# Performance work log

Measured on AMD Instinct MI355X. Metric: run time of the kernel, lower is better.

## Reference

```python
import math
import jax, jax.numpy as jnp
import numpy as np

B, D, T = 4, 512, 1024
H, DH, FF, K = 8, 64, 4, 31
NB, MD = 320, 800  # num_buckets, max_distance
ATTN_SCALE = 32.0


def setup_inputs() -> dict:
    key = jax.random.key(0)
    ks = jax.random.split(key, 16)
    n = lambda k, shape, s=0.02: jax.random.normal(k, shape, jnp.float32) * s
    return {
        "x": jax.random.normal(ks[0], (B, D, T), jnp.float32),
        "ff1_w1": n(ks[1], (D, FF * D)), "ff1_b1": jnp.zeros((FF * D,)),
        "ff1_w2": n(ks[2], (FF * D, D)), "ff1_b2": jnp.zeros((D,)),
        "qkv_w": n(ks[3], (D, 3 * D)), "qkv_b": jnp.zeros((3 * D,)),
        "out_w": n(ks[4], (D, D)), "out_b": jnp.zeros((D,)),
        "gn1_g": jnp.ones((D,)), "gn1_b": jnp.zeros((D,)),
        "pw1_w": n(ks[5], (D, 2 * D)), "pw1_b": jnp.zeros((2 * D,)),
        "dw_w": n(ks[6], (D, K)), "dw_b": jnp.zeros((D,)),
        "gn2_g": jnp.ones((D,)), "gn2_b": jnp.zeros((D,)),
        "pw2_w": n(ks[7], (D, D)), "pw2_b": jnp.zeros((D,)),
        "ff2_w1": n(ks[8], (D, FF * D)), "ff2_b1": jnp.zeros((FF * D,)),
        "ff2_w2": n(ks[9], (FF * D, D)), "ff2_b2": jnp.zeros((D,)),
        "rel_embed": n(ks[10], (NB, H), 1.0),
        "gate_u": n(ks[11], (H, DH)), "gate_w": n(ks[12], (H, DH)),
        "gate_scale": jnp.ones((H,)),
    }


def _rel_buckets(seq_len):
    # WavLM-style bucketization of relative positions (int, no grad).
    pos = jnp.arange(seq_len)
    rel = pos[None, :] - pos[:, None]                 # [T, T]
    half = NB // 2
    small = half // 2
    sign = (rel >= 0).astype(jnp.int32)
    a = jnp.abs(rel)
    is_small = a < small
    ac = jnp.maximum(a, 1)
    log_ratio = jnp.log(ac.astype(jnp.float32) / small) / math.log(MD / small)
    log_pos = small + (log_ratio * (half - small)).astype(jnp.int32)  # trunc toward 0, matches .long()
    log_pos = jnp.minimum(log_pos, half - 1)
    bucket = jnp.where(is_small, a, log_pos) + sign * half
    return jnp.clip(bucket, 0, NB - 1)


def _ffn(h, w1, b1, w2, b2):
    return jax.nn.gelu(h @ w1 + b1, approximate=False) @ w2 + b2


def _groupnorm1(h, g, b):  # GroupNorm(1, C) over [B, C, T]
    m = h.mean(axis=(1, 2), keepdims=True)
    v = h.var(axis=(1, 2), keepdims=True)
    return (h - m) / jnp.sqrt(v + 1e-5) * g[None, :, None] + b[None, :, None]


def reference(x, ff1_w1, ff1_b1, ff1_w2, ff1_b2, qkv_w, qkv_b, out_w, out_b,
              gn1_g, gn1_b, pw1_w, pw1_b, dw_w, dw_b, gn2_g, gn2_b, pw2_w, pw2_b,
              ff2_w1, ff2_b1, ff2_w2, ff2_b2, rel_embed, gate_u, gate_w, gate_scale):
    b_, d_, t_ = x.shape
    s = jnp.transpose(x, (0, 2, 1))                     # [B, T, D]
    s = s + 0.5 * _ffn(s, ff1_w1, ff1_b1, ff1_w2, ff1_b2)

    qkv = (s @ qkv_w + qkv_b).reshape(b_, t_, 3, H, DH)
    q = jnp.transpose(qkv[:, :, 0], (0, 2, 1, 3))       # [B, H, T, DH]
    k = jnp.transpose(qkv[:, :, 1], (0, 2, 1, 3))
    v = jnp.transpose(qkv[:, :, 2], (0, 2, 1, 3))

    scores = jnp.einsum('bhtd,bhsd->bhts', q / ATTN_SCALE, k)
    scores = (scores - scores.max(axis=-1, keepdims=True)) * ATTN_SCALE / math.sqrt(DH)

    # gated relative-position bias
    buckets = _rel_buckets(t_)                          # [T, T] int
    d = jnp.transpose(rel_embed[buckets], (2, 0, 1))[None]   # [1, H, T, T]
    g_upd = jax.nn.sigmoid(jnp.einsum('bhtd,hd->bht', q, gate_u))[..., None]
    g_rst = jax.nn.sigmoid(jnp.einsum('bhtd,hd->bht', q, gate_w))[..., None]
    r_tilde = gate_scale[None, :, None, None] * g_rst * d
    r = d + g_upd * d + (1 - g_upd) * r_tilde           # [B, H, T, T]

    probs = jax.nn.softmax(scores + r, axis=-1)
    attn = jnp.einsum('bhts,bhsd->bthd', probs, v).reshape(b_, t_, d_)
    s = s + attn @ out_w + out_b

    # conv module
    c = jnp.transpose(s, (0, 2, 1))                     # [B, D, T]
    h = _groupnorm1(c, gn1_g, gn1_b)
    h = jnp.einsum('bct,co->bot', h, pw1_w) + pw1_b[None, :, None]   # pointwise 1x1
    h_a, h_b = jnp.split(h, 2, axis=1)
    h = h_a * jax.nn.sigmoid(h_b)                       # GLU(dim=1)
    h = jax.lax.conv_general_dilated(
        h, dw_w[:, None, :], window_strides=(1,), padding=[(K // 2, K // 2)],
        dimension_numbers=('NCH', 'OIH', 'NCH'), feature_group_count=d_
    ) + dw_b[None, :, None]                             # depthwise conv
    h = _groupnorm1(h, gn2_g, gn2_b)
    h = jax.nn.silu(h)
    h = jnp.einsum('bct,co->bot', h, pw2_w) + pw2_b[None, :, None]
    c = c + h

    st = jnp.transpose(c, (0, 2, 1))
    st = st + 0.5 * _ffn(st, ff2_w1, ff2_b1, ff2_w2, ff2_b2)
    return jnp.transpose(st, (0, 2, 1))                 # [B, D, T]
```

## Files before the change

kernel.cpp:

```cpp
#include <hip/hip_runtime.h>
#include <hip/hip_bf16.h>
#include <math.h>

#define B_ 4
#define D_ 512
#define T_ 1024
#define H_ 8
#define FFD 2048

typedef unsigned short u16;
typedef short s16x8 __attribute__((ext_vector_type(8)));
typedef float f32x4 __attribute__((ext_vector_type(4)));

__device__ inline float sigm(float x){ return 1.f/(1.f+expf(-x)); }
__device__ inline float gelu_exact(float x){ return 0.5f*x*(1.f+erff(x*0.70710678118654752440f)); }
__device__ inline u16 f2b(float f){
  __hip_bfloat16 h = __float2bfloat16(f);
  return *reinterpret_cast<u16*>(&h);
}
__device__ inline float b2f(u16 u){ return __uint_as_float(((unsigned)u)<<16); }

__device__ inline void gl_lds16(const void* g, void* l) {
  __builtin_amdgcn_global_load_lds(
      (const __attribute__((address_space(1))) void*)g,
      (__attribute__((address_space(3))) void*)l, 16, 0, 0);
}

__global__ __launch_bounds__(256) void k_wt(const float* __restrict__ w, u16* __restrict__ wt, int K, int N) {
  __shared__ float tile[32][33];
  int n0 = blockIdx.x*32, k0 = blockIdx.y*32;
  int c = threadIdx.x & 31, r = threadIdx.x >> 5;
  for (int rr = r; rr < 32; rr += 8)
    tile[rr][c] = w[(size_t)(k0+rr)*N + n0 + c];
  __syncthreads();
  for (int rr = r; rr < 32; rr += 8)
    wt[(size_t)(n0+rr)*K + k0 + c] = f2b(tile[c][rr]);
}

__global__ __launch_bounds__(256) void k_wt_glu(const float* __restrict__ w, u16* __restrict__ wt, int K, int N) {
  __shared__ float tile[32][33];
  int n0 = blockIdx.x*32, k0 = blockIdx.y*32;
  int c = threadIdx.x & 31, r = threadIdx.x >> 5;
  for (int rr = r; rr < 32; rr += 8)
    tile[rr][c] = w[(size_t)(k0+rr)*N + n0 + c];
  __syncthreads();
  for (int rr = r; rr < 32; rr += 8) {
    int nr = n0 + rr;
    int np = (nr < 512) ? (nr*2) : ((nr-512)*2 + 1);
    wt[(size_t)np*K + k0 + c] = f2b(tile[c][rr]);
  }
}

__global__ void k_dwt(const float* __restrict__ w, float* __restrict__ wdt) {
  int idx = blockIdx.x*256 + threadIdx.x;
  if (idx < 31*512) {
    int k = idx >> 9, d = idx & 511;
    wdt[idx] = w[d*31 + k];
  }
}

__global__ __launch_bounds__(256) void k_xin(const float* __restrict__ x, float* __restrict__ sf, u16* __restrict__ sb) {
  __shared__ float tile[32][33];
  int b = blockIdx.z;
  int d0 = blockIdx.y * 32;
  int t0 = blockIdx.x * 32;
  int c = threadIdx.x & 31, r = threadIdx.x >> 5;
  for (int rr = r; rr < 32; rr += 8)
    tile[rr][c] = x[((size_t)(b*D_ + d0 + rr))*T_ + t0 + c];
  __syncthreads();
  for (int rr = r; rr < 32; rr += 8) {
    float v = tile[c][rr];
    size_t o = ((size_t)(b*T_ + t0 + rr))*D_ + d0 + c;
    sf[o] = v; sb[o] = f2b(v);
  }
}

__global__ __launch_bounds__(256) void k_transpose_out(const float* __restrict__ s, float* __restrict__ o) {
  __shared__ float tile[32][33];
  int b = blockIdx.z;
  int t0 = blockIdx.y * 32;
  int d0 = blockIdx.x * 32;
  int c = threadIdx.x & 31, r = threadIdx.x >> 5;
  for (int rr = r; rr < 32; rr += 8)
    tile[rr][c] = s[((size_t)(b*T_ + t0 + rr))*D_ + d0 + c];
  __syncthreads();
  for (int rr = r; rr < 32; rr += 8)
    o[((size_t)(b*D_ + d0 + rr))*T_ + t0 + c] = tile[c][rr];
}

template<int BM>
__global__ __launch_bounds__(256) void k_gemm_mfma(
    const u16* __restrict__ A, const u16* __restrict__ Wt,
    const float* __restrict__ bias, const float* __restrict__ res, float rscale,
    float* __restrict__ outf, u16* __restrict__ outb,
    u16* __restrict__ qd, u16* __restrict__ kd, u16* __restrict__ vd,
    u16* __restrict__ glub, float2* __restrict__ gnp, float* __restrict__ partf,
    int M, int N, int K, int kLen, int act)
{
  constexpr int MFR = BM/32;
  __shared__ u16 Ab[BM*64];
  __shared__ u16 Bb[128*64];
  int tid = threadIdx.x;
  int w = tid >> 6, lane = tid & 63;
  int lr = lane & 15, lk = lane >> 4;
  int wm = w >> 1, wn = w & 1;
  int m0 = blockIdx.y * BM, n0 = blockIdx.x * 128;
  int kbeg = partf ? blockIdx.z * kLen : 0;
  int kend = partf ? kbeg + kLen : K;
  f32x4 acc[MFR][4] = {};

  for (int kt = kbeg; kt < kend; kt += 64) {
    #pragma unroll
    for (int i = 0; i < MFR; ++i) {
      int slot = (w*MFR + i)*64 + lane;
      int r = slot >> 3, sc = slot & 7;
      int cc = sc ^ (r & 7);
      gl_lds16(A + (size_t)(m0 + r)*K + kt + cc*8, (char*)Ab + (size_t)(w*MFR+i)*1024);
    }
    #pragma unroll
    for (int i = 0; i < 4; ++i) {
      int slot = (w*4 + i)*64 + lane;
      int r = slot >> 3, sc = slot & 7;
      int cc = sc ^ (r & 7);
      gl_lds16(Wt + (size_t)(n0 + r)*K + kt + cc*8, (char*)Bb + (size_t)(w*4+i)*1024);
    }
    __syncthreads();
    #pragma unroll
    for (int ks = 0; ks < 2; ++ks) {
      s16x8 af[MFR], bfv[4];
      #pragma unroll
      for (int m = 0; m < MFR; ++m) {
        int r = wm*(BM/2) + m*16 + lr;
        int sl = (ks*4 + lk) ^ (r & 7);
        af[m] = *(const s16x8*)(Ab + r*64 + sl*8);
      }
      #pragma unroll
      for (int n = 0; n < 4; ++n) {
        int r = wn*64 + n*16 + lr;
        int sl = (ks*4 + lk) ^ (r & 7);
        bfv[n] = *(const s16x8*)(Bb + r*64 + sl*8);
      }
      #pragma unroll
      for (int m = 0; m < MFR; ++m)
        #pragma unroll
        for (int n = 0; n < 4; ++n)
          acc[m][n] = __builtin_amdgcn_mfma_f32_16x16x32_bf16(af[m], bfv[n], acc[m][n], 0, 0, 0);
    }
    __syncthreads();
  }

  if (partf) {
    float* pp = partf + (size_t)blockIdx.z * M * N;
    #pragma unroll
    for (int m = 0; m < MFR; ++m)
      #pragma unroll
      for (int n = 0; n < 4; ++n)
        #pragma unroll
        for (int r2 = 0; r2 < 4; ++r2) {
          int row = m0 + wm*(BM/2) + m*16 + lk*4 + r2;
          int col = n0 + wn*64 + n*16 + lr;
          pp[(size_t)row*N + col] = acc[m][n][r2];
        }
    return;
  }

  float psum = 0.f, psq = 0.f;
  #pragma unroll
  for (int m = 0; m < MFR; ++m) {
    #pragma unroll
    for (int n = 0; n < 4; ++n) {
      #pragma unroll
      for (int r2 = 0; r2 < 4; ++r2) {
        int row = m0 + wm*(BM/2) + m*16 + lk*4 + r2;
        int col = n0 + wn*64 + n*16 + lr;
        if (glub) {
          float vv = acc[m][n][r2] + bias[(col&1)*512 + (col>>1)];
          float pv = __shfl_xor(vv, 1);
          if ((col & 1) == 0)
            glub[(size_t)row*512 + (col>>1)] = f2b(vv * sigm(pv));
        } else {
          float vv = acc[m][n][r2] + bias[col];
          if (act) vv = gelu_exact(vv);
          size_t off = (size_t)row * N + col;
          if (res)  vv = res[off] + rscale * vv;
          if (outf) outf[off] = vv;
          if (outb) outb[off] = f2b(vv);
          if (qd) {
            int part = col >> 9, h = (col >> 6) & 7, dh = col & 63;
            int b = row >> 10, t = row & (T_-1);
            u16* dst = part == 0 ? qd : (part == 1 ? kd : vd);
            dst[(((size_t)(b*H_ + h))*T_ + t)*64 + dh] = f2b(vv);
          }
          psum += vv; psq += vv*vv;
        }
      }
    }
  }
  if (gnp) {
    float* r1 = (float*)Ab;
    float* r2s = (float*)Bb;
    __syncthreads();
    r1[tid] = psum; r2s[tid] = psq;
    __syncthreads();
    for (int off = 128; off; off >>= 1) {
      if (tid < off) { r1[tid] += r1[tid+off]; r2s[tid] += r2s[tid+off]; }
      __syncthreads();
    }
    if (tid == 0) {
      int bb = m0 >> 10;
      int mloc = (m0 >> (BM==64 ? 6 : 7)) & ((1024/BM) - 1);
      int idx = bb*(1024/BM)*4 + mloc*4 + (n0 >> 7);
      gnp[idx] = make_float2(r1[0], r2s[0]);
    }
  }
}

__global__ __launch_bounds__(256) void k_combine(
    const float4* __restrict__ p, const float* __restrict__ bias,
    const float4* __restrict__ res, float rscale,
    float4* __restrict__ outf, u16* __restrict__ outb)
{
  size_t i = (size_t)blockIdx.x*256 + threadIdx.x;
  int c4 = (i & 127) << 2;
  float4 a = p[i];
  float4 b = p[i + (size_t)(B_*T_)*128];
  float4 bs = *(const float4*)(bias + c4);
  float4 r = res[i];
  float4 v;
  v.x = r.x + rscale*(a.x + b.x + bs.x);
  v.y = r.y + rscale*(a.y + b.y + bs.y);
  v.z = r.z + rscale*(a.z + b.z + bs.z);
  v.w = r.w + rscale*(a.w + b.w + bs.w);
  if (outf) outf[i] = v;
  if (outb) {
    ushort4 u; u.x = f2b(v.x); u.y = f2b(v.y); u.z = f2b(v.z); u.w = f2b(v.w);
    *(ushort4*)(outb + i*4) = u;
  }
}

__global__ void k_rb(const float* __restrict__ rel_embed, float* __restrict__ rbg) {
  int idx = blockIdx.x*256 + threadIdx.x;
  int h = idx >> 11, j = idx & 2047;
  if (j >= 2047) { rbg[idx] = 0.f; return; }
  int rel = j - 1023;
  int sign = rel >= 0 ? 1 : 0;
  int a = rel >= 0 ? rel : -rel;
  int bkt;
  if (a < 80) bkt = a;
  else {
    float lr = logf((float)a / 80.f) / 2.30258509299404568402f;
    int lp = 80 + (int)(lr * 80.f);
    bkt = lp < 159 ? lp : 159;
  }
  bkt += sign*160;
  rbg[idx] = rel_embed[bkt*H_ + h];
}

__global__ __launch_bounds__(256) void k_vt(const u16* __restrict__ vb, u16* __restrict__ vtb) {
  __shared__ u16 tl[64][65];
  int blk = blockIdx.x;
  int tt0 = (blk & 15) * 64;
  size_t bh = (size_t)(blk >> 4);
  int tid = threadIdx.x;
  #pragma unroll
  for (int i = 0; i < 4; ++i) {
    int idx = i*256 + tid;
    int t = idx >> 4, d0 = (idx & 15) * 4;
    *(ushort4*)&tl[t][d0] = *(const ushort4*)(vb + (bh*T_ + tt0 + t)*64 + d0);
  }
  __syncthreads();
  #pragma unroll
  for (int i = 0; i < 4; ++i) {
    int idx = i*256 + tid;
    int dh = idx >> 4, t4 = (idx & 15) * 4;
    ushort4 o;
    o.x = tl[t4+0][dh]; o.y = tl[t4+1][dh]; o.z = tl[t4+2][dh]; o.w = tl[t4+3][dh];
    *(ushort4*)(vtb + (bh*64 + dh)*T_ + tt0 + t4) = o;
  }
}

__global__ __launch_bounds__(256) void k_attn3(
    const u16* __restrict__ qb, const u16* __restrict__ kb, const u16* __restrict__ vtb,
    const float* __restrict__ rbg,
    const float* __restrict__ gu, const float* __restrict__ gw, const float* __restrict__ gs,
    u16* __restrict__ outb)
{
  __shared__ u16 Kl[64*64];
  __shared__ u16 Vtl[64*64];
  __shared__ u16 Pl[64*64];
  __shared__ float rb[2048];
  __shared__ float cf[64];
  int blk = blockIdx.x;
  int qt = blk & 15;
  int h  = (blk >> 4) & 7;
  int b  = blk >> 7;
  int tid = threadIdx.x;
  int w = tid >> 6, lane = tid & 63;
  int lr = lane & 15, lk = lane >> 4;
  int g = lane >> 4;
  int t0 = qt * 64;
  size_t bh = (size_t)(b*H_ + h);

  for (int j = tid; j < 2048; j += 256) rb[j] = rbg[h*2048 + j];
  if (tid < 64) {
    const u16* qrow = qb + (bh*T_ + t0 + tid)*64;
    float vu = 0.f, vw = 0.f;
    for (int kk2 = 0; kk2 < 64; ++kk2) {
      float qv = b2f(qrow[kk2]);
      vu += qv * gu[h*64+kk2];
      vw += qv * gw[h*64+kk2];
    }
    float g1 = sigm(vu), g2 = sigm(vw);
    cf[tid] = 1.f + g1 + (1.f-g1)*gs[h]*g2;
  }
  const u16* qbase = qb + (bh*T_ + t0 + w*16 + lr)*64;
  s16x8 qa0 = *(const s16x8*)(qbase + lk*8);
  s16x8 qa1 = *(const s16x8*)(qbase + 32 + lk*8);

  f32x4 O[4] = {};
  float mcur[4] = {-1e30f,-1e30f,-1e30f,-1e30f};
  float lsum[4] = {0.f,0.f,0.f,0.f};
  const f32x4 zero = {0.f,0.f,0.f,0.f};
  __syncthreads();

  for (int kt = 0; kt < 16; ++kt) {
    #pragma unroll
    for (int i = 0; i < 2; ++i) {
      int slot = (i*4 + w)*64 + lane;
      int r = slot >> 3, scc = slot & 7;
      int cc = scc ^ (r & 7);
      gl_lds16(kb  + (bh*T_ + kt*64 + r)*64 + cc*8, (char*)Kl  + (i*4+w)*1024);
      gl_lds16(vtb + (bh*64 + r)*T_ + kt*64 + cc*8, (char*)Vtl + (i*4+w)*1024);
    }
    __syncthreads();
    f32x4 sc[4];
    #pragma unroll
    for (int n = 0; n < 4; ++n) {
      int row = n*16 + lr;
      int c0 = (0*4 + lk) ^ (row & 7);
      int c1 = (1*4 + lk) ^ (row & 7);
      s16x8 kb0 = *(const s16x8*)(Kl + row*64 + c0*8);
      s16x8 kb1 = *(const s16x8*)(Kl + row*64 + c1*8);
      f32x4 t = __builtin_amdgcn_mfma_f32_16x16x32_bf16(qa0, kb0, zero, 0, 0, 0);
      sc[n]   = __builtin_amdgcn_mfma_f32_16x16x32_bf16(qa1, kb1, t, 0, 0, 0);
    }
    float tmax[4];
    #pragma unroll
    for (int r2 = 0; r2 < 4; ++r2) {
      int q_local = w*16 + g*4 + r2;
      float cfv = cf[q_local];
      int qabs = t0 + q_local;
      float mx = -1e30f;
      #pragma unroll
      for (int n = 0; n < 4; ++n) {
        int sabs = kt*64 + n*16 + lr;
        float v = sc[n][r2]*0.125f + cfv * rb[sabs - qabs + 1023];
        sc[n][r2] = v;
        mx = fmaxf(mx, v);
      }
      tmax[r2] = mx;
    }
    #pragma unroll
    for (int mk = 1; mk < 16; mk <<= 1)
      #pragma unroll
      for (int r2 = 0; r2 < 4; ++r2)
        tmax[r2] = fmaxf(tmax[r2], __shfl_xor(tmax[r2], mk));
    float scl[4], psum[4];
    #pragma unroll
    for (int r2 = 0; r2 < 4; ++r2) {
      float mnew = fmaxf(mcur[r2], tmax[r2]);
      scl[r2] = __expf(mcur[r2] - mnew);
      mcur[r2] = mnew;
      int q_local = w*16 + g*4 + r2;
      float ps = 0.f;
      #pragma unroll
      for (int n = 0; n < 4; ++n) {
        float e = __expf(sc[n][r2] - mnew);
        ps += e;
        int s_local = n*16 + lr;
        Pl[q_local*64 + (((s_local>>3) ^ (q_local&7))<<3) + (s_local&7)] = f2b(e);
      }
      psum[r2] = ps;
    }
    #pragma unroll
    for (int mk = 1; mk < 16; mk <<= 1)
      #pragma unroll
      for (int r2 = 0; r2 < 4; ++r2)
        psum[r2] += __shfl_xor(psum[r2], mk);
    #pragma unroll
    for (int r2 = 0; r2 < 4; ++r2) lsum[r2] = lsum[r2]*scl[r2] + psum[r2];
    #pragma unroll
    for (int n = 0; n < 4; ++n)
      #pragma unroll
      for (int r2 = 0; r2 < 4; ++r2)
        O[n][r2] *= scl[r2];
    __syncthreads();
    int qrow = w*16 + lr;
    int pc0 = (0*4 + lk) ^ (qrow & 7), pc1 = (1*4 + lk) ^ (qrow & 7);
    s16x8 pa0 = *(const s16x8*)(Pl + qrow*64 + pc0*8);
    s16x8 pa1 = *(const s16x8*)(Pl + qrow*64 + pc1*8);
    #pragma unroll
    for (int n = 0; n < 4; ++n) {
      int dh = n*16 + lr;
      int c0 = (0*4 + lk) ^ (dh & 7), c1 = (1*4 + lk) ^ (dh & 7);
      s16x8 vb0 = *(const s16x8*)(Vtl + dh*64 + c0*8);
      s16x8 vb1 = *(const s16x8*)(Vtl + dh*64 + c1*8);
      O[n] = __builtin_amdgcn_mfma_f32_16x16x32_bf16(pa0, vb0, O[n], 0, 0, 0);
      O[n] = __builtin_amdgcn_mfma_f32_16x16x32_bf16(pa1, vb1, O[n], 0, 0, 0);
    }
    __syncthreads();
  }
  float inv[4];
  #pragma unroll
  for (int r2 = 0; r2 < 4; ++r2) inv[r2] = 1.f / lsum[r2];
  #pragma unroll
  for (int n = 0; n < 4; ++n)
    #pragma unroll
    for (int r2 = 0; r2 < 4; ++r2) {
      int q = t0 + w*16 + g*4 + r2;
      int dh = n*16 + lr;
      outb[((size_t)(b*T_) + q)*512 + h*64 + dh] = f2b(O[n][r2]*inv[r2]);
    }
}

__global__ __launch_bounds__(256) void k_dwconv2(
    const u16* __restrict__ g, const float* __restrict__ wdt,
    const float* __restrict__ bias, float* __restrict__ o, float2* __restrict__ part)
{
  int b = blockIdx.z, tg = blockIdx.y;
  int ch = blockIdx.x*256 + threadIdx.x;
  int t0 = tg*16;
  float wk[31];
  #pragma unroll
  for (int k = 0; k < 31; ++k) wk[k] = wdt[k*512 + ch];
  float win[46];
  const u16* gb = g + ((size_t)b*T_)*512 + ch;
  #pragma unroll
  for (int j = 0; j < 46; ++j) {
    int tt = t0 + j - 15;
    win[j] = (tt >= 0 && tt < T_) ? b2f(gb[(size_t)tt*512]) : 0.f;
  }
  float bv = bias[ch];
  float bsum = 0.f, bsq = 0.f;
  float* ob = o + ((size_t)b*T_ + t0)*512 + ch;
  #pragma unroll
  for (int j = 0; j < 16; ++j) {
    float acc = bv;
    #pragma unroll
    for (int k = 0; k < 31; ++k) acc += win[j+k]*wk[k];
    ob[(size_t)j*512] = acc;
    bsum += acc; bsq += acc*acc;
  }
  __shared__ float rs[256], rq[256];
  rs[threadIdx.x] = bsum; rq[threadIdx.x] = bsq; __syncthreads();
  for (int off = 128; off; off >>= 1) {
    if (threadIdx.x < off) { rs[threadIdx.x] += rs[threadIdx.x+off]; rq[threadIdx.x] += rq[threadIdx.x+off]; }
    __syncthreads();
  }
  if (threadIdx.x == 0) part[b*128 + tg*2 + blockIdx.x] = make_float2(rs[0], rq[0]);
}

__global__ void k_gn_final(const float2* __restrict__ part, float2* __restrict__ stats, int n) {
  int b = blockIdx.x;
  float s = 0.f, s2 = 0.f;
  for (int i = threadIdx.x; i < n; i += 64) {
    float2 p = part[b*n + i];
    s += p.x; s2 += p.y;
  }
  for (int off = 32; off; off >>= 1) { s += __shfl_down(s, off); s2 += __shfl_down(s2, off); }
  if (threadIdx.x == 0) {
    float cnt = (float)(D_*T_);
    float mean = s/cnt;
    float var = s2/cnt - mean*mean;
    stats[b] = make_float2(mean, rsqrtf(var + 1e-5f));
  }
}

__global__ void k_gn_apply(const float* __restrict__ x, const float2* __restrict__ stats,
                           const float* __restrict__ g, const float* __restrict__ bta,
                           u16* __restrict__ o, int silu_flag)
{
  size_t idx = (size_t)blockIdx.x*256 + threadIdx.x;
  int dd = idx & (D_-1);
  int b = (int)(idx >> 19);
  float2 st = stats[b];
  float v = (x[idx]-st.x)*st.y*g[dd] + bta[dd];
  if (silu_flag) v = v*sigm(v);
  o[idx] = f2b(v);
}

extern "C" void kernel_launch(void* const* d_in, const int* in_sizes, int n_in,
                              void* d_out, int out_size, void* d_ws, size_t ws_size,
                              hipStream_t stream)
{
  const float* x      = (const float*)d_in[0];
  const float* ff1_w1 = (const float*)d_in[1];
  const float* ff1_b1 = (const float*)d_in[2];
  const float* ff1_w2 = (const float*)d_in[3];
  const float* ff1_b2 = (const float*)d_in[4];
  const float* qkv_w  = (const float*)d_in[5];
  const float* qkv_b  = (const float*)d_in[6];
  const float* out_w  = (const float*)d_in[7];
  const float* out_b  = (const float*)d_in[8];
  const float* gn1_g  = (const float*)d_in[9];
  const float* gn1_b  = (const float*)d_in[10];
  const float* pw1_w  = (const float*)d_in[11];
  const float* pw1_b  = (const float*)d_in[12];
  const float* dw_w   = (const float*)d_in[13];
  const float* dw_b   = (const float*)d_in[14];
  const float* gn2_g  = (const float*)d_in[15];
  const float* gn2_b  = (const float*)d_in[16];
  const float* pw2_w  = (const float*)d_in[17];
  const float* pw2_b  = (const float*)d_in[18];
  const float* ff2_w1 = (const float*)d_in[19];
  const float* ff2_b1 = (const float*)d_in[20];
  const float* ff2_w2 = (const float*)d_in[21];
  const float* ff2_b2 = (const float*)d_in[22];
  const float* rel_embed = (const float*)d_in[23];
  const float* gate_u = (const float*)d_in[24];
  const float* gate_w = (const float*)d_in[25];
  const float* gate_scale = (const float*)d_in[26];

  char* ws = (char*)d_ws;
  const size_t MB = (size_t)1 << 20;
  float* s0f  = (float*)(ws + 0*MB);
  u16*   s0b  = (u16*)  (ws + 8*MB);
  u16*   h1b  = (u16*)  (ws + 12*MB);
  float* Sf   = (float*)(ws + 28*MB);
  u16*   Sb   = (u16*)  (ws + 36*MB);
  u16*   qbb  = (u16*)  (ws + 40*MB);
  u16*   kbb  = (u16*)  (ws + 44*MB);
  u16*   vbb  = (u16*)  (ws + 48*MB);
  u16*   vtb  = (u16*)  (ws + 52*MB);
  float* S2f  = (float*)(ws + 0*MB);
  u16*   attb = (u16*)  (ws + 8*MB);
  u16*   gn1b = (u16*)  (ws + 36*MB);
  u16*   glub = (u16*)  (ws + 56*MB);
  float* dcf  = (float*)(ws + 28*MB);
  u16*   gn2b = (u16*)  (ws + 36*MB);
  float* S3f  = (float*)(ws + 40*MB);
  u16*   S3b  = (u16*)  (ws + 48*MB);
  u16*   h3b  = (u16*)  (ws + 12*MB);
  float* Sout = (float*)(ws + 28*MB);
  float* PK1  = (float*)(ws + 40*MB);
  float* PK2  = (float*)(ws + 48*MB);
  u16* ff1w1t = (u16*)(ws + 64*MB);
  u16* ff1w2t = (u16*)(ws + 66*MB);
  u16* qkvt   = (u16*)(ws + 68*MB);
  u16* outt   = (u16*)(ws + 70*MB);
  u16* pw1t   = (u16*)(ws + 72*MB);
  u16* pw2t   = (u16*)(ws + 74*MB);
  u16* ff2w1t = (u16*)(ws + 76*MB);
  u16* ff2w2t = (u16*)(ws + 78*MB);
  float* rbg  = (float*)(ws + 80*MB);
  float* wdt  = (float*)(ws + 81*MB);
  float2* part1 = (float2*)(ws + 84*MB);
  float2* part2 = (float2*)(ws + 84*MB + 8192);
  float2* st1   = (float2*)(ws + 84*MB + 16384);
  float2* st2   = (float2*)(ws + 84*MB + 16384 + 64);

  const int M = B_*T_;
  dim3 blk(256);

  k_wt<<<dim3(FFD/32, D_/32), blk, 0, stream>>>(ff1_w1, ff1w1t, D_, FFD);
  k_wt<<<dim3(D_/32, FFD/32), blk, 0, stream>>>(ff1_w2, ff1w2t, FFD, D_);
  k_wt<<<dim3(1536/32, D_/32), blk, 0, stream>>>(qkv_w, qkvt, D_, 1536);
  k_wt<<<dim3(D_/32, D_/32), blk, 0, stream>>>(out_w, outt, D_, D_);
  k_wt_glu<<<dim3(1024/32, D_/32), blk, 0, stream>>>(pw1_w, pw1t, D_, 1024);
  k_wt<<<dim3(D_/32, D_/32), blk, 0, stream>>>(pw2_w, pw2t, D_, D_);
  k_wt<<<dim3(FFD/32, D_/32), blk, 0, stream>>>(ff2_w1, ff2w1t, D_, FFD);
  k_wt<<<dim3(D_/32, FFD/32), blk, 0, stream>>>(ff2_w2, ff2w2t, FFD, D_);
  k_rb<<<dim3(64), blk, 0, stream>>>(rel_embed, rbg);
  k_dwt<<<dim3(62), blk, 0, stream>>>(dw_w, wdt);

  k_xin<<<dim3(T_/32, D_/32, B_), blk, 0, stream>>>(x, s0f, s0b);

  k_gemm_mfma<128><<<dim3(FFD/128, M/128), blk, 0, stream>>>(s0b, ff1w1t, ff1_b1, nullptr, 0.f,
      nullptr, h1b, nullptr, nullptr, nullptr, nullptr, nullptr, nullptr, M, FFD, D_, 0, 1);
  k_gemm_mfma<64><<<dim3(D_/128, M/64, 2), blk, 0, stream>>>(h1b, ff1w2t, nullptr, nullptr, 0.f,
      nullptr, nullptr, nullptr, nullptr, nullptr, nullptr, nullptr, PK1, M, D_, FFD, 1024, 0);
  k_combine<<<dim3((M*128)/256), blk, 0, stream>>>((const float4*)PK1, ff1_b2, (const float4*)s0f, 0.5f,
      (float4*)Sf, Sb);
  k_gemm_mfma<64><<<dim3(1536/128, M/64), blk, 0, stream>>>(Sb, qkvt, qkv_b, nullptr, 0.f,
      nullptr, nullptr, qbb, kbb, vbb, nullptr, nullptr, nullptr, M, 1536, D_, 0, 0);
  k_vt<<<dim3(B_*H_*16), blk, 0, stream>>>(vbb, vtb);
  k_attn3<<<dim3(B_*H_*16), blk, 0, stream>>>(qbb, kbb, vtb, rbg, gate_u, gate_w, gate_scale, attb);
  k_gemm_mfma<64><<<dim3(D_/128, M/64), blk, 0, stream>>>(attb, outt, out_b, Sf, 1.f,
      S2f, nullptr, nullptr, nullptr, nullptr, nullptr, part1, nullptr, M, D_, D_, 0, 0);
  k_gn_final<<<dim3(B_), dim3(64), 0, stream>>>(part1, st1, 64);
  k_gn_apply<<<dim3((M*D_)/256), blk, 0, stream>>>(S2f, st1, gn1_g, gn1_b, gn1b, 0);
  k_gemm_mfma<64><<<dim3(1024/128, M/64), blk, 0, stream>>>(gn1b, pw1t, pw1_b, nullptr, 0.f,
      nullptr, nullptr, nullptr, nullptr, nullptr, glub, nullptr, nullptr, M, 1024, D_, 0, 0);
  k_dwconv2<<<dim3(2, T_/16, B_), blk, 0, stream>>>(glub, wdt, dw_b, dcf, part2);
  k_gn_final<<<dim3(B_), dim3(64), 0, stream>>>(part2, st2, 128);
  k_gn_apply<<<dim3((M*D_)/256), blk, 0, stream>>>(dcf, st2, gn2_g, gn2_b, gn2b, 1);
  k_gemm_mfma<64><<<dim3(D_/128, M/64), blk, 0, stream>>>(gn2b, pw2t, pw2_b, S2f, 1.f,
      S3f, S3b, nullptr, nullptr, nullptr, nullptr, nullptr, nullptr, M, D_, D_, 0, 0);
  k_gemm_mfma<128><<<dim3(FFD/128, M/128), blk, 0, stream>>>(S3b, ff2w1t, ff2_b1, nullptr, 0.f,
      nullptr, h3b, nullptr, nullptr, nullptr, nullptr, nullptr, nullptr, M, FFD, D_, 0, 1);
  k_gemm_mfma<64><<<dim3(D_/128, M/64, 2), blk, 0, stream>>>(h3b, ff2w2t, nullptr, nullptr, 0.f,
      nullptr, nullptr, nullptr, nullptr, nullptr, nullptr, nullptr, PK2, M, D_, FFD, 1024, 0);
  k_combine<<<dim3((M*128)/256), blk, 0, stream>>>((const float4*)PK2, ff2_b2, (const float4*)S3f, 0.5f,
      (float4*)Sout, nullptr);
  k_transpose_out<<<dim3(D_/32, T_/32, B_), blk, 0, stream>>>(Sout, (float*)d_out);
}
```

Baseline: 439.3 us.

## Merge prep kernels, fold GN finalize into apply, use 64x64 GEMM tiles

Eleven setup launches (weight transposes, relative-bias table, depthwise weight transpose, input transpose) are merged into a single k_prep kernel that dispatches on block index. The two GroupNorm finalize kernels are removed, and every k_gn_apply block now reduces the 128 partial stats itself, which repeats that small reduction in each block. The smaller GEMMs move from 64x128 to 64x64 tiles, doubling the grid to fill more CUs at the cost of less operand reuse per block.

```diff
diff --git a/kernel.cpp b/kernel.cpp
--- a/kernel.cpp
+++ b/kernel.cpp
@@ -26,53 +26,93 @@
       (__attribute__((address_space(3))) void*)l, 16, 0, 0);
 }
 
-__global__ __launch_bounds__(256) void k_wt(const float* __restrict__ w, u16* __restrict__ wt, int K, int N) {
-  __shared__ float tile[32][33];
-  int n0 = blockIdx.x*32, k0 = blockIdx.y*32;
-  int c = threadIdx.x & 31, r = threadIdx.x >> 5;
-  for (int rr = r; rr < 32; rr += 8)
-    tile[rr][c] = w[(size_t)(k0+rr)*N + n0 + c];
-  __syncthreads();
-  for (int rr = r; rr < 32; rr += 8)
-    wt[(size_t)(n0+rr)*K + k0 + c] = f2b(tile[c][rr]);
-}
-
-__global__ __launch_bounds__(256) void k_wt_glu(const float* __restrict__ w, u16* __restrict__ wt, int K, int N) {
-  __shared__ float tile[32][33];
-  int n0 = blockIdx.x*32, k0 = blockIdx.y*32;
+__device__ void wt_tile(const float* __restrict__ w, u16* __restrict__ wt,
+                        int K, int N, int nxb, int kyb, float (*tile)[33], bool glu) {
+  int n0 = nxb*32, k0 = kyb*32;
   int c = threadIdx.x & 31, r = threadIdx.x >> 5;
   for (int rr = r; rr < 32; rr += 8)
     tile[rr][c] = w[(size_t)(k0+rr)*N + n0 + c];
   __syncthreads();
   for (int rr = r; rr < 32; rr += 8) {
     int nr = n0 + rr;
-    int np = (nr < 512) ? (nr*2) : ((nr-512)*2 + 1);
+    int np = glu ? ((nr < 512) ? nr*2 : (nr-512)*2 + 1) : nr;
     wt[(size_t)np*K + k0 + c] = f2b(tile[c][rr]);
   }
 }
 
-__global__ void k_dwt(const float* __restrict__ w, float* __restrict__ wdt) {
-  int idx = blockIdx.x*256 + threadIdx.x;
-  if (idx < 31*512) {
-    int k = idx >> 9, d = idx & 511;
-    wdt[idx] = w[d*31 + k];
-  }
-}
-
-__global__ __launch_bounds__(256) void k_xin(const float* __restrict__ x, float* __restrict__ sf, u16* __restrict__ sb) {
-  __shared__ float tile[32][33];
-  int b = blockIdx.z;
-  int d0 = blockIdx.y * 32;
-  int t0 = blockIdx.x * 32;
+__device__ void xin_tile(const float* __restrict__ x, float* __restrict__ sf, u16* __restrict__ sb,
+                         int tb, int db, int bb, float (*tile)[33]) {
+  int d0 = db*32, t0 = tb*32;
   int c = threadIdx.x & 31, r = threadIdx.x >> 5;
   for (int rr = r; rr < 32; rr += 8)
-    tile[rr][c] = x[((size_t)(b*D_ + d0 + rr))*T_ + t0 + c];
+    tile[rr][c] = x[((size_t)(bb*D_ + d0 + rr))*T_ + t0 + c];
   __syncthreads();
   for (int rr = r; rr < 32; rr += 8) {
     float v = tile[c][rr];
-    size_t o = ((size_t)(b*T_ + t0 + rr))*D_ + d0 + c;
+    size_t o = ((size_t)(bb*T_ + t0 + rr))*D_ + d0 + c;
     sf[o] = v; sb[o] = f2b(v);
   }
+}
+
+__global__ __launch_bounds__(256) void k_prep(
+    const float* __restrict__ x,
+    const float* __restrict__ ff1_w1, const float* __restrict__ ff1_w2,
+    const float* __restrict__ qkv_w, const float* __restrict__ out_w,
+    const float* __restrict__ pw1_w, const float* __restrict__ pw2_w,
+    const float* __restrict__ ff2_w1, const float* __restrict__ ff2_w2,
+    const float* __restrict__ rel_embed, const float* __restrict__ dw_w,
+    float* __restrict__ s0f, u16* __restrict__ s0b,
+    u16* ff1w1t, u16* ff1w2t, u16* qkvt, u16* outt, u16* pw1t, u16* pw2t,
+    u16* ff2w1t, u16* ff2w2t, float* __restrict__ rbg, float* __restrict__ wdt)
+{
+  __shared__ float tile[32][33];
+  int bid = blockIdx.x;
+  if (bid < 1024) { wt_tile(ff1_w1, ff1w1t, 512, 2048, bid%64, bid/64, tile, false); return; }
+  bid -= 1024;
+  if (bid < 1024) { wt_tile(ff1_w2, ff1w2t, 2048, 512, bid%16, bid/16, tile, false); return; }
+  bid -= 1024;
+  if (bid < 768)  { wt_tile(qkv_w, qkvt, 512, 1536, bid%48, bid/48, tile, false); return; }
+  bid -= 768;
+  if (bid < 256)  { wt_tile(out_w, outt, 512, 512, bid%16, bid/16, tile, false); return; }
+  bid -= 256;
+  if (bid < 512)  { wt_tile(pw1_w, pw1t, 512, 1024, bid%32, bid/32, tile, true); return; }
+  bid -= 512;
+  if (bid < 256)  { wt_tile(pw2_w, pw2t, 512, 512, bid%16, bid/16, tile, false); return; }
+  bid -= 256;
+  if (bid < 1024) { wt_tile(ff2_w1, ff2w1t, 512, 2048, bid%64, bid/64, tile, false); return; }
+  bid -= 1024;
+  if (bid < 1024) { wt_tile(ff2_w2, ff2w2t, 2048, 512, bid%16, bid/16, tile, false); return; }
+  bid -= 1024;
+  if (bid < 64) {
+    int idx = bid*256 + threadIdx.x;
+    int h = idx >> 11, j = idx & 2047;
+    if (j >= 2047) { rbg[idx] = 0.f; return; }
+    int rel = j - 1023;
+    int sign = rel >= 0 ? 1 : 0;
+    int a = rel >= 0 ? rel : -rel;
+    int bkt;
+    if (a < 80) bkt = a;
+    else {
+      float lr = logf((float)a / 80.f) / 2.30258509299404568402f;
+      int lp = 80 + (int)(lr * 80.f);
+      bkt = lp < 159 ? lp : 159;
+    }
+    bkt += sign*160;
+    rbg[idx] = rel_embed[bkt*H_ + h];
+    return;
+  }
+  bid -= 64;
+  if (bid < 62) {
+    int idx = bid*256 + threadIdx.x;
+    if (idx < 31*512) {
+      int k = idx >> 9, d = idx & 511;
+      wdt[idx] = dw_w[d*31 + k];
+    }
+    return;
+  }
+  bid -= 62;
+  int tb = bid & 31, db = (bid >> 5) & 15, bb = bid >> 9;
+  xin_tile(x, s0f, s0b, tb, db, bb, tile);
 }
 
 __global__ __launch_bounds__(256) void k_transpose_out(const float* __restrict__ s, float* __restrict__ o) {
@@ -88,7 +128,7 @@
     o[((size_t)(b*D_ + d0 + rr))*T_ + t0 + c] = tile[c][rr];
 }
 
-template<int BM>
+template<int BM, int BN>
 __global__ __launch_bounds__(256) void k_gemm_mfma(
     const u16* __restrict__ A, const u16* __restrict__ Wt,
     const float* __restrict__ bias, const float* __restrict__ res, float rscale,
@@ -97,17 +137,17 @@
     u16* __restrict__ glub, float2* __restrict__ gnp, float* __restrict__ partf,
     int M, int N, int K, int kLen, int act)
 {
-  constexpr int MFR = BM/32;
+  constexpr int MFR = BM/32, NFR = BN/32;
   __shared__ u16 Ab[BM*64];
-  __shared__ u16 Bb[128*64];
+  __shared__ u16 Bb[BN*64];
   int tid = threadIdx.x;
   int w = tid >> 6, lane = tid & 63;
   int lr = lane & 15, lk = lane >> 4;
   int wm = w >> 1, wn = w & 1;
-  int m0 = blockIdx.y * BM, n0 = blockIdx.x * 128;
+  int m0 = blockIdx.y * BM, n0 = blockIdx.x * BN;
   int kbeg = partf ? blockIdx.z * kLen : 0;
   int kend = partf ? kbeg + kLen : K;
-  f32x4 acc[MFR][4] = {};
+  f32x4 acc[MFR][NFR] = {};
 
   for (int kt = kbeg; kt < kend; kt += 64) {
     #pragma unroll
@@ -118,16 +158,16 @@
       gl_lds16(A + (size_t)(m0 + r)*K + kt + cc*8, (char*)Ab + (size_t)(w*MFR+i)*1024);
     }
     #pragma unroll
-    for (int i = 0; i < 4; ++i) {
-      int slot = (w*4 + i)*64 + lane;
+    for (int i = 0; i < NFR; ++i) {
+      int slot = (w*NFR + i)*64 + lane;
       int r = slot >> 3, sc = slot & 7;
       int cc = sc ^ (r & 7);
-      gl_lds16(Wt + (size_t)(n0 + r)*K + kt + cc*8, (char*)Bb + (size_t)(w*4+i)*1024);
+      gl_lds16(Wt + (size_t)(n0 + r)*K + kt + cc*8, (char*)Bb + (size_t)(w*NFR+i)*1024);
     }
     __syncthreads();
     #pragma unroll
     for (int ks = 0; ks < 2; ++ks) {
-      s16x8 af[MFR], bfv[4];
+      s16x8 af[MFR], bfv[NFR];
       #pragma unroll
       for (int m = 0; m < MFR; ++m) {
         int r = wm*(BM/2) + m*16 + lr;
@@ -135,15 +175,15 @@
         af[m] = *(const s16x8*)(Ab + r*64 + sl*8);
       }
       #pragma unroll
-      for (int n = 0; n < 4; ++n) {
-        int r = wn*64 + n*16 + lr;
+      for (int n = 0; n < NFR; ++n) {
+        int r = wn*(BN/2) + n*16 + lr;
         int sl = (ks*4 + lk) ^ (r & 7);
         bfv[n] = *(const s16x8*)(Bb + r*64 + sl*8);
       }
       #pragma unroll
       for (int m = 0; m < MFR; ++m)
         #pragma unroll
-        for (int n = 0; n < 4; ++n)
+        for (int n = 0; n < NFR; ++n)
           acc[m][n] = __builtin_amdgcn_mfma_f32_16x16x32_bf16(af[m], bfv[n], acc[m][n], 0, 0, 0);
     }
     __syncthreads();
@@ -154,11 +194,11 @@
     #pragma unroll
     for (int m = 0; m < MFR; ++m)
       #pragma unroll
-      for (int n = 0; n < 4; ++n)
+      for (int n = 0; n < NFR; ++n)
         #pragma unroll
         for (int r2 = 0; r2 < 4; ++r2) {
           int row = m0 + wm*(BM/2) + m*16 + lk*4 + r2;
-          int col = n0 + wn*64 + n*16 + lr;
+          int col = n0 + wn*(BN/2) + n*16 + lr;
           pp[(size_t)row*N + col] = acc[m][n][r2];
         }
     return;
@@ -168,11 +208,11 @@
   #pragma unroll
   for (int m = 0; m < MFR; ++m) {
     #pragma unroll
-    for (int n = 0; n < 4; ++n) {
+    for (int n = 0; n < NFR; ++n) {
       #pragma unroll
       for (int r2 = 0; r2 < 4; ++r2) {
         int row = m0 + wm*(BM/2) + m*16 + lk*4 + r2;
-        int col = n0 + wn*64 + n*16 + lr;
+        int col = n0 + wn*(BN/2) + n*16 + lr;
         if (glub) {
           float vv = acc[m][n][r2] + bias[(col&1)*512 + (col>>1)];
           float pv = __shfl_xor(vv, 1);
@@ -208,9 +248,9 @@
     }
     if (tid == 0) {
       int bb = m0 >> 10;
-      int mloc = (m0 >> (BM==64 ? 6 : 7)) & ((1024/BM) - 1);
-      int idx = bb*(1024/BM)*4 + mloc*4 + (n0 >> 7);
-      gnp[idx] = make_float2(r1[0], r2s[0]);
+      int mpb = 1024/BM, nb = N/BN;
+      int mloc = (m0/BM) & (mpb - 1);
+      gnp[bb*mpb*nb + mloc*nb + n0/BN] = make_float2(r1[0], r2s[0]);
     }
   }
 }
@@ -236,24 +276,6 @@
     ushort4 u; u.x = f2b(v.x); u.y = f2b(v.y); u.z = f2b(v.z); u.w = f2b(v.w);
     *(ushort4*)(outb + i*4) = u;
   }
-}
-
-__global__ void k_rb(const float* __restrict__ rel_embed, float* __restrict__ rbg) {
-  int idx = blockIdx.x*256 + threadIdx.x;
-  int h = idx >> 11, j = idx & 2047;
-  if (j >= 2047) { rbg[idx] = 0.f; return; }
-  int rel = j - 1023;
-  int sign = rel >= 0 ? 1 : 0;
-  int a = rel >= 0 ? rel : -rel;
-  int bkt;
-  if (a < 80) bkt = a;
-  else {
-    float lr = logf((float)a / 80.f) / 2.30258509299404568402f;
-    int lp = 80 + (int)(lr * 80.f);
-    bkt = lp < 159 ? lp : 159;
-  }
-  bkt += sign*160;
-  rbg[idx] = rel_embed[bkt*H_ + h];
 }
 
 __global__ __launch_bounds__(256) void k_vt(const u16* __restrict__ vb, u16* __restrict__ vtb) {
@@ -460,31 +482,33 @@
   if (threadIdx.x == 0) part[b*128 + tg*2 + blockIdx.x] = make_float2(rs[0], rq[0]);
 }
 
-__global__ void k_gn_final(const float2* __restrict__ part, float2* __restrict__ stats, int n) {
-  int b = blockIdx.x;
+__global__ __launch_bounds__(256) void k_gn_apply(
+    const float* __restrict__ x, const float2* __restrict__ part, int np,
+    const float* __restrict__ g, const float* __restrict__ bta,
+    u16* __restrict__ o, int silu_flag)
+{
+  __shared__ float rs[256], rq[256];
+  __shared__ float2 stat;
+  size_t idx = (size_t)blockIdx.x*256 + threadIdx.x;
+  int b = (int)(idx >> 19);
   float s = 0.f, s2 = 0.f;
-  for (int i = threadIdx.x; i < n; i += 64) {
-    float2 p = part[b*n + i];
-    s += p.x; s2 += p.y;
-  }
-  for (int off = 32; off; off >>= 1) { s += __shfl_down(s, off); s2 += __shfl_down(s2, off); }
+  for (int i = threadIdx.x; i < np; i += 256) {
+    float2 p = part[b*np + i]; s += p.x; s2 += p.y;
+  }
+  rs[threadIdx.x] = s; rq[threadIdx.x] = s2; __syncthreads();
+  for (int off = 128; off; off >>= 1) {
+    if (threadIdx.x < off) { rs[threadIdx.x] += rs[threadIdx.x+off]; rq[threadIdx.x] += rq[threadIdx.x+off]; }
+    __syncthreads();
+  }
   if (threadIdx.x == 0) {
     float cnt = (float)(D_*T_);
-    float mean = s/cnt;
-    float var = s2/cnt - mean*mean;
-    stats[b] = make_float2(mean, rsqrtf(var + 1e-5f));
-  }
-}
-
-__global__ void k_gn_apply(const float* __restrict__ x, const float2* __restrict__ stats,
-                           const float* __restrict__ g, const float* __restrict__ bta,
-                           u16* __restrict__ o, int silu_flag)
-{
-  size_t idx = (size_t)blockIdx.x*256 + threadIdx.x;
+    float mean = rs[0]/cnt;
+    float var = rq[0]/cnt - mean*mean;
+    stat = make_float2(mean, rsqrtf(var + 1e-5f));
+  }
+  __syncthreads();
   int dd = idx & (D_-1);
-  int b = (int)(idx >> 19);
-  float2 st = stats[b];
-  float v = (x[idx]-st.x)*st.y*g[dd] + bta[dd];
+  float v = (x[idx]-stat.x)*stat.y*g[dd] + bta[dd];
   if (silu_flag) v = v*sigm(v);
   o[idx] = f2b(v);
 }
@@ -556,49 +580,36 @@
   float* wdt  = (float*)(ws + 81*MB);
   float2* part1 = (float2*)(ws + 84*MB);
   float2* part2 = (float2*)(ws + 84*MB + 8192);
-  float2* st1   = (float2*)(ws + 84*MB + 16384);
-  float2* st2   = (float2*)(ws + 84*MB + 16384 + 64);
 
   const int M = B_*T_;
   dim3 blk(256);
 
-  k_wt<<<dim3(FFD/32, D_/32), blk, 0, stream>>>(ff1_w1, ff1w1t, D_, FFD);
-  k_wt<<<dim3(D_/32, FFD/32), blk, 0, stream>>>(ff1_w2, ff1w2t, FFD, D_);
-  k_wt<<<dim3(1536/32, D_/32), blk, 0, stream>>>(qkv_w, qkvt, D_, 1536);
-  k_wt<<<dim3(D_/32, D_/32), blk, 0, stream>>>(out_w, outt, D_, D_);
-  k_wt_glu<<<dim3(1024/32, D_/32), blk, 0, stream>>>(pw1_w, pw1t, D_, 1024);
-  k_wt<<<dim3(D_/32, D_/32), blk, 0, stream>>>(pw2_w, pw2t, D_, D_);
-  k_wt<<<dim3(FFD/32, D_/32), blk, 0, stream>>>(ff2_w1, ff2w1t, D_, FFD);
-  k_wt<<<dim3(D_/32, FFD/32), blk, 0, stream>>>(ff2_w2, ff2w2t, FFD, D_);
-  k_rb<<<dim3(64), blk, 0, stream>>>(rel_embed, rbg);
-  k_dwt<<<dim3(62), blk, 0, stream>>>(dw_w, wdt);
-
-  k_xin<<<dim3(T_/32, D_/32, B_), blk, 0, stream>>>(x, s0f, s0b);
-
-  k_gemm_mfma<128><<<dim3(FFD/128, M/128), blk, 0, stream>>>(s0b, ff1w1t, ff1_b1, nullptr, 0.f,
+  k_prep<<<dim3(8062), blk, 0, stream>>>(x, ff1_w1, ff1_w2, qkv_w, out_w, pw1_w, pw2_w,
+      ff2_w1, ff2_w2, rel_embed, dw_w, s0f, s0b,
+      ff1w1t, ff1w2t, qkvt, outt, pw1t, pw2t, ff2w1t, ff2w2t, rbg, wdt);
+
+  k_gemm_mfma<128,128><<<dim3(FFD/128, M/128), blk, 0, stream>>>(s0b, ff1w1t, ff1_b1, nullptr, 0.f,
       nullptr, h1b, nullptr, nullptr, nullptr, nullptr, nullptr, nullptr, M, FFD, D_, 0, 1);
-  k_gemm_mfma<64><<<dim3(D_/128, M/64, 2), blk, 0, stream>>>(h1b, ff1w2t, nullptr, nullptr, 0.f,
+  k_gemm_mfma<64,64><<<dim3(D_/64, M/64, 2), blk, 0, stream>>>(h1b, ff1w2t, nullptr, nullptr, 0.f,
       nullptr, nullptr, nullptr, nullptr, nullptr, nullptr, nullptr, PK1, M, D_, FFD, 1024, 0);
   k_combine<<<dim3((M*128)/256), blk, 0, stream>>>((const float4*)PK1, ff1_b2, (const float4*)s0f, 0.5f,
       (float4*)Sf, Sb);
-  k_gemm_mfma<64><<<dim3(1536/128, M/64), blk, 0, stream>>>(Sb, qkvt, qkv_b, nullptr, 0.f,
+  k_gemm_mfma<64,64><<<dim3(1536/64, M/64), blk, 0, stream>>>(Sb, qkvt, qkv_b, nullptr, 0.f,
       nullptr, nullptr, qbb, kbb, vbb, nullptr, nullptr, nullptr, M, 1536, D_, 0, 0);
   k_vt<<<dim3(B_*H_*16), blk, 0, stream>>>(vbb, vtb);
   k_attn3<<<dim3(B_*H_*16), blk, 0, stream>>>(qbb, kbb, vtb, rbg, gate_u, gate_w, gate_scale, attb);
-  k_gemm_mfma<64><<<dim3(D_/128, M/64), blk, 0, stream>>>(attb, outt, out_b, Sf, 1.f,
+  k_gemm_mfma<64,64><<<dim3(D_/64, M/64), blk, 0, stream>>>(attb, outt, out_b, Sf, 1.f,
       S2f, nullptr, nullptr, nullptr, nullptr, nullptr, part1, nullptr, M, D_, D_, 0, 0);
-  k_gn_final<<<dim3(B_), dim3(64), 0, stream>>>(part1, st1, 64);
-  k_gn_apply<<<dim3((M*D_)/256), blk, 0, stream>>>(S2f, st1, gn1_g, gn1_b, gn1b, 0);
-  k_gemm_mfma<64><<<dim3(1024/128, M/64), blk, 0, stream>>>(gn1b, pw1t, pw1_b, nullptr, 0.f,
+  k_gn_apply<<<dim3((M*D_)/256), blk, 0, stream>>>(S2f, part1, 128, gn1_g, gn1_b, gn1b, 0);
+  k_gemm_mfma<64,64><<<dim3(1024/64, M/64), blk, 0, stream>>>(gn1b, pw1t, pw1_b, nullptr, 0.f,
       nullptr, nullptr, nullptr, nullptr, nullptr, glub, nullptr, nullptr, M, 1024, D_, 0, 0);
   k_dwconv2<<<dim3(2, T_/16, B_), blk, 0, stream>>>(glub, wdt, dw_b, dcf, part2);
-  k_gn_final<<<dim3(B_), dim3(64), 0, stream>>>(part2, st2, 128);
-  k_gn_apply<<<dim3((M*D_)/256), blk, 0, stream>>>(dcf, st2, gn2_g, gn2_b, gn2b, 1);
-  k_gemm_mfma<64><<<dim3(D_/128, M/64), blk, 0, stream>>>(gn2b, pw2t, pw2_b, S2f, 1.f,
+  k_gn_apply<<<dim3((M*D_)/256), blk, 0, stream>>>(dcf, part2, 128, gn2_g, gn2_b, gn2b, 1);
+  k_gemm_mfma<64,64><<<dim3(D_/64, M/64), blk, 0, stream>>>(gn2b, pw2t, pw2_b, S2f, 1.f,
       S3f, S3b, nullptr, nullptr, nullptr, nullptr, nullptr, nullptr, M, D_, D_, 0, 0);
-  k_gemm_mfma<128><<<dim3(FFD/128, M/128), blk, 0, stream>>>(S3b, ff2w1t, ff2_b1, nullptr, 0.f,
+  k_gemm_mfma<128,128><<<dim3(FFD/128, M/128), blk, 0, stream>>>(S3b, ff2w1t, ff2_b1, nullptr, 0.f,
       nullptr, h3b, nullptr, nullptr, nullptr, nullptr, nullptr, nullptr, M, FFD, D_, 0, 1);
-  k_gemm_mfma<64><<<dim3(D_/128, M/64, 2), blk, 0, stream>>>(h3b, ff2w2t, nullptr, nullptr, 0.f,
+  k_gemm_mfma<64,64><<<dim3(D_/64, M/64, 2), blk, 0, stream>>>(h3b, ff2w2t, nullptr, nullptr, 0.f,
       nullptr, nullptr, nullptr, nullptr, nullptr, nullptr, nullptr, PK2, M, D_, FFD, 1024, 0);
   k_combine<<<dim3((M*128)/256), blk, 0, stream>>>((const float4*)PK2, ff2_b2, (const float4*)S3f, 0.5f,
       (float4*)Sout, nullptr);
```

Result: faster. 399.3 us (-9.1%).
